# Kernel tuning notes

Hardware: AMD Instinct MI355X
Metric: run time of the kernel (lower is better)

## Reference

```python
import jax, jax.numpy as jnp
import numpy as np

DATA_DIM = 784
MANIFOLD_DIM = 16
HIDDEN = 256
BATCH = 131072


def setup_inputs() -> dict:
    key = jax.random.key(0)
    ks = jax.random.split(key, 10)
    s = lambda fan_in: 1.0 / np.sqrt(fan_in)
    return {
        "x_t": jax.random.normal(ks[0], (BATCH, DATA_DIM), dtype=jnp.float32),
        "t": jax.random.uniform(ks[1], (BATCH,), dtype=jnp.float32),
        # metric_net: Linear(784,256) -> ReLU -> Linear(256, 16*16)
        "W1": jax.random.uniform(ks[2], (DATA_DIM, HIDDEN), jnp.float32, -s(DATA_DIM), s(DATA_DIM)),
        "b1": jax.random.uniform(ks[3], (HIDDEN,), jnp.float32, -s(DATA_DIM), s(DATA_DIM)),
        "W2": jax.random.uniform(ks[4], (HIDDEN, MANIFOLD_DIM * MANIFOLD_DIM), jnp.float32, -s(HIDDEN), s(HIDDEN)),
        "b2": jax.random.uniform(ks[5], (MANIFOLD_DIM * MANIFOLD_DIM,), jnp.float32, -s(HIDDEN), s(HIDDEN)),
        # project_to_manifold: Linear(784, 16)
        "Wp": jax.random.uniform(ks[6], (DATA_DIM, MANIFOLD_DIM), jnp.float32, -s(DATA_DIM), s(DATA_DIM)),
        "bp": jax.random.uniform(ks[7], (MANIFOLD_DIM,), jnp.float32, -s(DATA_DIM), s(DATA_DIM)),
        # lift_from_manifold: Linear(16, 784)
        "Wl": jax.random.uniform(ks[8], (MANIFOLD_DIM, DATA_DIM), jnp.float32, -s(MANIFOLD_DIM), s(MANIFOLD_DIM)),
        "bl": jax.random.uniform(ks[9], (DATA_DIM,), jnp.float32, -s(MANIFOLD_DIM), s(MANIFOLD_DIM)),
    }


def reference(x_t, t, W1, b1, W2, b2, Wp, bp, Wl, bl):
    d = MANIFOLD_DIM
    # project_to_manifold
    xi = x_t @ Wp + bp  # [B, d]
    # metric_tensor: g = A A^T + 0.1 I, A = metric_net(x).reshape(B, d, d)
    h = jax.nn.relu(x_t @ W1 + b1)
    g_flat = h @ W2 + b2
    A = g_flat.reshape(-1, d, d)
    g = jnp.einsum('bik,bjk->bij', A, A) + 0.1 * jnp.eye(d, dtype=x_t.dtype)
    g_inv = jnp.linalg.inv(g)  # batched small 16x16 inverse
    # latent score: -xi / (t + eps)
    latent_score = -xi / (t[:, None] + 1e-6)
    riemannian_score = jnp.einsum('bij,bj->bi', g_inv, latent_score)
    score_data = riemannian_score @ Wl + bl  # [B, 784]
    return score_data
```

## Files before the change

### kernel.cpp

```cpp
#include <hip/hip_runtime.h>

typedef __attribute__((ext_vector_type(8))) short short8;
typedef __attribute__((ext_vector_type(4))) float f32x4;

#define NT   256
#define ROWS 32

#define W1T_PL  435200
#define W1T_COL 1600
#define W2T_OFF 870400
#define W2T_PL  131072
#define W2T_COL 512
#define WLT_OFF 1132544
#define WLT_PL  25088
#define WLT_COL 32

#define OFF_W0   0
#define OFF_W1   34816
#define OFF_H    34816
#define OFF_X0   69632
#define OFF_X1   73728
#define OFF_XIP  69632
#define OFF_YS   77824
#define LDS_SZ   79872

#define MFMA16(a,b,c) __builtin_amdgcn_mfma_f32_16x16x32_bf16(a,b,c,0,0,0)

__device__ __forceinline__ unsigned short bf16_rn(float x){
  unsigned u = __float_as_uint(x);
  return (unsigned short)((u + 0x7fffu + ((u >> 16) & 1u)) >> 16);
}
__device__ __forceinline__ float bf16f(unsigned short h){
  return __uint_as_float(((unsigned)h) << 16);
}

__device__ __forceinline__ void glds16(const void* g, void* s){
#if __has_builtin(__builtin_amdgcn_global_load_lds)
  __builtin_amdgcn_global_load_lds((const __attribute__((address_space(1))) void*)g,
                                   (__attribute__((address_space(3))) void*)s, 16, 0, 0);
#else
  const int lane = (int)(threadIdx.x & 63u);
  *(short8*)((char*)s + lane*16) = *(const short8*)((const char*)g);
#endif
}

__global__ __launch_bounds__(256)
void prep_w(const float* __restrict__ W1, const float* __restrict__ W2,
            const float* __restrict__ Wp, const float* __restrict__ Wl,
            unsigned short* __restrict__ ws)
{
  const int u = blockIdx.x * 256 + threadIdx.x;
  float v[8];
  int bh, blo;
  if (u < 27200) {
    int kg = u / 272, col = u - kg*272;
    #pragma unroll
    for (int j = 0; j < 8; ++j) {
      int k = kg*8 + j;
      v[j] = (k < 784) ? ((col < 256) ? W1[k*256 + col] : Wp[k*16 + (col-256)]) : 0.0f;
    }
    bh = col*800 + kg*8; blo = bh + 217600;
  } else if (u < 35392) {
    int q = u - 27200;
    int kg = q >> 8, col = q & 255;
    #pragma unroll
    for (int j = 0; j < 8; ++j) v[j] = W2[(kg*8+j)*256 + col];
    bh = 435200 + col*256 + kg*8; blo = bh + 65536;
  } else if (u < 36960) {
    int q = u - 35392;
    int kg = (q >= 784) ? 1 : 0; int col = q - kg*784;
    #pragma unroll
    for (int j = 0; j < 8; ++j) v[j] = Wl[(kg*8+j)*784 + col];
    bh = 566272 + col*16 + kg*8; blo = bh + 12544;
  } else return;
  short8 hv, lv;
  #pragma unroll
  for (int j = 0; j < 8; ++j) {
    unsigned short hh = bf16_rn(v[j]);
    hv[j] = (short)hh;
    lv[j] = (short)bf16_rn(v[j] - bf16f(hh));
  }
  *(short8*)&ws[bh]  = hv;
  *(short8*)&ws[blo] = lv;
}

__global__ __launch_bounds__(NT, 2)
void riemann_mfma(const float* __restrict__ x, const float* __restrict__ tvec,
                  const float* __restrict__ b1g, const float* __restrict__ b2g,
                  const float* __restrict__ bpg, const float* __restrict__ blg,
                  const char* __restrict__ wst, float* __restrict__ out)
{
  __shared__ __align__(16) char lds[LDS_SZ];
  const int tid = threadIdx.x;
  const int wv  = tid >> 6;
  const int l   = tid & 63;
  const int lr  = l & 15;
  const int lg  = l >> 4;
  const int row0 = (int)blockIdx.x * ROWS;

  const f32x4 Z4 = {0.f, 0.f, 0.f, 0.f};
  const short8 Z8 = {0,0,0,0,0,0,0,0};

  f32x4 acc[2][4];
  f32x4 xia[2];
  #pragma unroll
  for (int mt = 0; mt < 2; ++mt) {
    xia[mt] = Z4;
    #pragma unroll
    for (int nt = 0; nt < 4; ++nt) acc[mt][nt] = Z4;
  }

  const int xrow = tid >> 3;
  const int kq   = tid & 7;
  const int xwoff = xrow*64 + (((kq>>1) ^ ((xrow>>1)&3))<<4) + (kq&1)*8;

  auto loadX = [&](int ct)->f32x4 {
    f32x4 v = Z4;
    if (ct < 25) {
      int kb = ct*32 + kq*4;
      if (kb < 784) v = *(const f32x4*)(x + (long)(row0 + xrow)*784 + kb);
    }
    return v;
  };
  auto writeX = [&](const f32x4& xv, int slot){
    unsigned long long hq = 0, lq = 0;
    #pragma unroll
    for (int e = 0; e < 4; ++e) {
      unsigned short hh = bf16_rn(xv[e]);
      unsigned short ll = bf16_rn(xv[e] - bf16f(hh));
      hq |= ((unsigned long long)hh) << (16*e);
      lq |= ((unsigned long long)ll) << (16*e);
    }
    char* b = lds + (slot ? OFF_X1 : OFF_X0) + xwoff;
    *(unsigned long long*)b = hq;
    *(unsigned long long*)(b + 2048) = lq;
  };
  auto stageW1 = [&](int t, int slot){
    #pragma unroll
    for (int i2 = 0; i2 < 9; ++i2) {
      int i = wv + i2*4;
      if (i < 34) {
        int f = i*64 + l;
        int pl = (f >= 1088) ? 1 : 0;
        int r  = f - pl*1088;
        int col = r >> 2, kgp = r & 3;
        glds16(wst + pl*W1T_PL + col*W1T_COL + t*64 + ((kgp ^ ((col>>1)&3)) << 4),
               lds + (slot ? OFF_W1 : OFF_W0) + i*1024);
      }
    }
  };

  f32x4 xv0 = loadX(0);
  stageW1(0, 0);
  writeX(xv0, 0);
  f32x4 xv = loadX(1);
  __syncthreads();

  for (int t = 0; t < 25; ++t) {
    const int cur = t & 1, nxt = cur ^ 1;
    if (t < 24) {
      stageW1(t + 1, nxt);
      writeX(xv, nxt);
      xv = loadX(t + 2);
    }
    const char* Xb = lds + (cur ? OFF_X1 : OFF_X0);
    const char* Wb = lds + (cur ? OFF_W1 : OFF_W0);

    short8 af[2][2];
    #pragma unroll
    for (int mt = 0; mt < 2; ++mt) {
      int row = mt*16 + lr;
      int sl = lg ^ ((row>>1)&3);
      af[0][mt] = *(const short8*)(Xb +        row*64 + sl*16);
      af[1][mt] = *(const short8*)(Xb + 2048 + row*64 + sl*16);
    }
    short8 bfr[2][4];
    #pragma unroll
    for (int nt = 0; nt < 4; ++nt) {
      int col = wv*64 + nt*16 + lr;
      int sl = lg ^ ((col>>1)&3);
      bfr[0][nt] = *(const short8*)(Wb +         col*64 + sl*16);
      bfr[1][nt] = *(const short8*)(Wb + 17408 + col*64 + sl*16);
    }
    #pragma unroll
    for (int mt = 0; mt < 2; ++mt)
      #pragma unroll
      for (int nt = 0; nt < 4; ++nt) {
        acc[mt][nt] = MFMA16(af[0][mt], bfr[0][nt], acc[mt][nt]);
        acc[mt][nt] = MFMA16(af[0][mt], bfr[1][nt], acc[mt][nt]);
        acc[mt][nt] = MFMA16(af[1][mt], bfr[0][nt], acc[mt][nt]);
      }
    if ((t & 3) == wv) {
      int colx = 256 + lr;
      int slx = lg ^ ((colx>>1)&3);
      short8 bx0 = *(const short8*)(Wb +         colx*64 + slx*16);
      short8 bx1 = *(const short8*)(Wb + 17408 + colx*64 + slx*16);
      #pragma unroll
      for (int mt = 0; mt < 2; ++mt) {
        xia[mt] = MFMA16(af[0][mt], bx0, xia[mt]);
        xia[mt] = MFMA16(af[0][mt], bx1, xia[mt]);
        xia[mt] = MFMA16(af[1][mt], bx0, xia[mt]);
      }
    }
    __syncthreads();
  }

  {
    #pragma unroll
    for (int i2 = 0; i2 < 8; ++i2) {
      int i = wv + i2*4;
      int f = i*64 + l;
      int pl = f >> 10, r = f & 1023;
      int col = r >> 2, kgp = r & 3;
      glds16(wst + W2T_OFF + pl*W2T_PL + col*W2T_COL + 0*64 + ((kgp ^ ((col>>1)&3)) << 4),
             lds + OFF_W0 + i*1024);
    }
  }
  #pragma unroll
  for (int nt = 0; nt < 4; ++nt) {
    int col = wv*64 + nt*16 + lr;
    float b1v = b1g[col];
    #pragma unroll
    for (int mt = 0; mt < 2; ++mt)
      #pragma unroll
      for (int r = 0; r < 4; ++r) {
        int row = mt*16 + lg*4 + r;
        float v = acc[mt][nt][r] + b1v;
        v = v > 0.f ? v : 0.f;
        unsigned short hh = bf16_rn(v);
        unsigned short ll = bf16_rn(v - bf16f(hh));
        int bo = (row*512 + col*2) ^ ((row&7)<<4);
        *(unsigned short*)(lds + OFF_H +         bo) = hh;
        *(unsigned short*)(lds + OFF_H + 16384 + bo) = ll;
      }
  }
  #pragma unroll
  for (int mt = 0; mt < 2; ++mt)
    #pragma unroll
    for (int r = 0; r < 4; ++r) {
      int row = mt*16 + lg*4 + r;
      *(float*)(lds + OFF_XIP + wv*2048 + row*64 + lr*4) = xia[mt][r];
    }
  __syncthreads();

  f32x4 ac2[2][4];
  #pragma unroll
  for (int mt = 0; mt < 2; ++mt)
    #pragma unroll
    for (int nt = 0; nt < 4; ++nt) ac2[mt][nt] = Z4;

  for (int t = 0; t < 8; ++t) {
    short8 ah[2], alo[2];
    #pragma unroll
    for (int mt = 0; mt < 2; ++mt) {
      int row = mt*16 + lr;
      int bo = (row*512 + t*64 + lg*16) ^ ((row&7)<<4);
      ah[mt]  = *(const short8*)(lds + OFF_H +         bo);
      alo[mt] = *(const short8*)(lds + OFF_H + 16384 + bo);
    }
    short8 b2f[2][4];
    #pragma unroll
    for (int nt = 0; nt < 4; ++nt) {
      int col = wv*64 + nt*16 + lr;
      int sl = lg ^ ((col>>1)&3);
      b2f[0][nt] = *(const short8*)(lds + OFF_W0 +         col*64 + sl*16);
      b2f[1][nt] = *(const short8*)(lds + OFF_W0 + 16384 + col*64 + sl*16);
    }
    __syncthreads();
    if (t < 7) {
      #pragma unroll
      for (int i2 = 0; i2 < 8; ++i2) {
        int i = wv + i2*4;
        int f = i*64 + l;
        int pl = f >> 10, r = f & 1023;
        int col = r >> 2, kgp = r & 3;
        glds16(wst + W2T_OFF + pl*W2T_PL + col*W2T_COL + (t+1)*64 + ((kgp ^ ((col>>1)&3)) << 4),
               lds + OFF_W0 + i*1024);
      }
    }
    #pragma unroll
    for (int mt = 0; mt < 2; ++mt)
      #pragma unroll
      for (int nt = 0; nt < 4; ++nt) {
        ac2[mt][nt] = MFMA16(ah[mt],  b2f[0][nt], ac2[mt][nt]);
        ac2[mt][nt] = MFMA16(ah[mt],  b2f[1][nt], ac2[mt][nt]);
        ac2[mt][nt] = MFMA16(alo[mt], b2f[0][nt], ac2[mt][nt]);
      }
    __syncthreads();
  }
  #pragma unroll
  for (int nt = 0; nt < 4; ++nt) {
    int col = wv*64 + nt*16 + lr;
    float b2v = b2g[col];
    #pragma unroll
    for (int mt = 0; mt < 2; ++mt)
      #pragma unroll
      for (int r = 0; r < 4; ++r) {
        int row = mt*16 + lg*4 + r;
        *(float*)(lds + OFF_W0 + row*1024 + col*4) = ac2[mt][nt][r] + b2v;
      }
  }
  __syncthreads();

  const int grp = tid >> 4;
  const int j16 = tid & 15;
  float aA[16], aB[16];
  {
    const char* g0 = lds + OFF_W0 + grp*1024 + j16*64;
    const char* g1 = lds + OFF_W0 + (16+grp)*1024 + j16*64;
    *(f32x4*)&aA[0]  = *(const f32x4*)(g0);
    *(f32x4*)&aA[4]  = *(const f32x4*)(g0 + 16);
    *(f32x4*)&aA[8]  = *(const f32x4*)(g0 + 32);
    *(f32x4*)&aA[12] = *(const f32x4*)(g0 + 48);
    *(f32x4*)&aB[0]  = *(const f32x4*)(g1);
    *(f32x4*)&aB[4]  = *(const f32x4*)(g1 + 16);
    *(f32x4*)&aB[8]  = *(const f32x4*)(g1 + 32);
    *(f32x4*)&aB[12] = *(const f32x4*)(g1 + 48);
  }
  float bpv = bpg[j16];
  float xs0 = *(const float*)(lds + OFF_XIP +        grp*64 + j16*4)
            + *(const float*)(lds + OFF_XIP + 2048 + grp*64 + j16*4)
            + *(const float*)(lds + OFF_XIP + 4096 + grp*64 + j16*4)
            + *(const float*)(lds + OFF_XIP + 6144 + grp*64 + j16*4) + bpv;
  float xs1 = *(const float*)(lds + OFF_XIP +        (16+grp)*64 + j16*4)
            + *(const float*)(lds + OFF_XIP + 2048 + (16+grp)*64 + j16*4)
            + *(const float*)(lds + OFF_XIP + 4096 + (16+grp)*64 + j16*4)
            + *(const float*)(lds + OFF_XIP + 6144 + (16+grp)*64 + j16*4) + bpv;
  float rhs0 = -xs0 / (tvec[row0 + grp] + 1e-6f);
  float rhs1 = -xs1 / (tvec[row0 + 16 + grp] + 1e-6f);
  __syncthreads();

  {
    #pragma unroll
    for (int i2 = 0; i2 < 13; ++i2) {
      int i = wv + i2*4;
      if (i < 49) {
        int f = i*64 + l;
        int pl = (f >= 1568) ? 1 : 0;
        int r  = f - pl*1568;
        int col = r >> 1, kg = r & 1;
        glds16(wst + WLT_OFF + pl*WLT_PL + col*WLT_COL + kg*16,
               lds + OFF_W0 + i*1024);
      }
    }
  }
  {
    float rw[16];
    #pragma unroll
    for (int i = 0; i < 16; ++i) {
      float d = (i == j16) ? 0.1f : 0.0f;
      #pragma unroll
      for (int k = 0; k < 16; ++k) d += aA[k] * __shfl(aA[k], i, 16);
      rw[i] = d;
    }
    float rdv = 0.f;
    #pragma unroll
    for (int k = 0; k < 16; ++k) {
      float piv = __shfl(rw[k], k, 16);
      float rp = 1.0f / piv;
      float f = rw[k] * rp;
      f = (j16 == k) ? 0.0f : f;
      if (j16 == k) rdv = rp;
      #pragma unroll
      for (int q = k+1; q < 16; ++q)
        rw[q] -= f * __shfl(rw[q], k, 16);
      rhs0 -= f * __shfl(rhs0, k, 16);
    }
    float y = rhs0 * rdv;
    unsigned short yh = bf16_rn(y);
    unsigned short yl = bf16_rn(y - bf16f(yh));
    *(unsigned short*)(lds + OFF_YS +        grp*32 + j16*2) = yh;
    *(unsigned short*)(lds + OFF_YS + 1024 + grp*32 + j16*2) = yl;
  }
  {
    float rw[16];
    #pragma unroll
    for (int i = 0; i < 16; ++i) {
      float d = (i == j16) ? 0.1f : 0.0f;
      #pragma unroll
      for (int k = 0; k < 16; ++k) d += aB[k] * __shfl(aB[k], i, 16);
      rw[i] = d;
    }
    float rdv = 0.f;
    #pragma unroll
    for (int k = 0; k < 16; ++k) {
      float piv = __shfl(rw[k], k, 16);
      float rp = 1.0f / piv;
      float f = rw[k] * rp;
      f = (j16 == k) ? 0.0f : f;
      if (j16 == k) rdv = rp;
      #pragma unroll
      for (int q = k+1; q < 16; ++q)
        rw[q] -= f * __shfl(rw[q], k, 16);
      rhs1 -= f * __shfl(rhs1, k, 16);
    }
    float y = rhs1 * rdv;
    unsigned short yh = bf16_rn(y);
    unsigned short yl = bf16_rn(y - bf16f(yh));
    *(unsigned short*)(lds + OFF_YS +        (16+grp)*32 + j16*2) = yh;
    *(unsigned short*)(lds + OFF_YS + 1024 + (16+grp)*32 + j16*2) = yl;
  }
  __syncthreads();

  short8 ya[2][2];
  #pragma unroll
  for (int p = 0; p < 2; ++p)
    #pragma unroll
    for (int mt = 0; mt < 2; ++mt) {
      short8 v = Z8;
      if (lg < 2) v = *(const short8*)(lds + OFF_YS + p*1024 + (mt*16 + lr)*32 + lg*16);
      ya[p][mt] = v;
    }

  for (int nt = wv; nt < 49; nt += 4) {
    short8 w0 = Z8, w1v = Z8;
    if (lg < 2) {
      int col = nt*16 + lr;
      w0  = *(const short8*)(lds + OFF_W0 +         col*32 + lg*16);
      w1v = *(const short8*)(lds + OFF_W0 + 25088 + col*32 + lg*16);
    }
    float blv = blg[nt*16 + lr];
    #pragma unroll
    for (int mt = 0; mt < 2; ++mt) {
      f32x4 a5 = Z4;
      a5 = MFMA16(ya[0][mt], w0,  a5);
      a5 = MFMA16(ya[0][mt], w1v, a5);
      a5 = MFMA16(ya[1][mt], w0,  a5);
      #pragma unroll
      for (int r = 0; r < 4; ++r)
        out[(long)(row0 + mt*16 + lg*4 + r)*784 + nt*16 + lr] = a5[r] + blv;
    }
  }
}

extern "C" void kernel_launch(void* const* d_in, const int* in_sizes, int n_in,
                              void* d_out, int out_size, void* d_ws, size_t ws_size,
                              hipStream_t stream)
{
  (void)n_in; (void)out_size; (void)ws_size;
  const float* x  = (const float*)d_in[0];
  const float* t  = (const float*)d_in[1];
  const float* W1 = (const float*)d_in[2];
  const float* b1 = (const float*)d_in[3];
  const float* W2 = (const float*)d_in[4];
  const float* b2 = (const float*)d_in[5];
  const float* Wp = (const float*)d_in[6];
  const float* bp = (const float*)d_in[7];
  const float* Wl = (const float*)d_in[8];
  const float* bl = (const float*)d_in[9];
  float* out = (float*)d_out;
  const int B = in_sizes[1];

  hipLaunchKernelGGL(prep_w, dim3(145), dim3(256), 0, stream,
                     W1, W2, Wp, Wl, (unsigned short*)d_ws);
  hipLaunchKernelGGL(riemann_mfma, dim3(B / ROWS), dim3(NT), 0, stream,
                     x, t, b1, b2, bp, bl, (const char*)d_ws, out);
}
```

Before: 1.089 ms.

## Double block to 512 threads with explicit waitcnt/barrier pipelining and priority hints

Raises the workgroup to 8 waves, halving each wave's N-slice in both GEMM phases, splitting X loads into float2 per thread, and giving each thread one 16x16 solve instead of two. __syncthreads is replaced with manual vmcnt/lgkmcnt waits plus s_barrier so async global->LDS weight staging can stay in flight across iterations. MFMA sections are wrapped in s_setprio. The aim is more latency hiding and less per-thread serial solve work. The risks are wrong hand-counted vmcnt values and more barrier overhead.

```diff
diff --git a/kernel.cpp b/kernel.cpp
--- a/kernel.cpp
+++ b/kernel.cpp
@@ -2,8 +2,9 @@
 
 typedef __attribute__((ext_vector_type(8))) short short8;
 typedef __attribute__((ext_vector_type(4))) float f32x4;
-
-#define NT   256
+typedef __attribute__((ext_vector_type(2))) float f32x2;
+
+#define NT   512
 #define ROWS 32
 
 #define W1T_PL  435200
@@ -25,6 +26,9 @@
 #define LDS_SZ   79872
 
 #define MFMA16(a,b,c) __builtin_amdgcn_mfma_f32_16x16x32_bf16(a,b,c,0,0,0)
+#define WAITV(N) asm volatile("s_waitcnt vmcnt(" #N ")" ::: "memory")
+#define WAITL()  asm volatile("s_waitcnt lgkmcnt(0)" ::: "memory")
+#define SBAR()   __builtin_amdgcn_s_barrier()
 
 __device__ __forceinline__ unsigned short bf16_rn(float x){
   unsigned u = __float_as_uint(x);
@@ -84,7 +88,7 @@
   *(short8*)&ws[blo] = lv;
 }
 
-__global__ __launch_bounds__(NT, 2)
+__global__ __launch_bounds__(NT, 4)
 void riemann_mfma(const float* __restrict__ x, const float* __restrict__ tvec,
                   const float* __restrict__ b1g, const float* __restrict__ b2g,
                   const float* __restrict__ bpg, const float* __restrict__ blg,
@@ -101,44 +105,42 @@
   const f32x4 Z4 = {0.f, 0.f, 0.f, 0.f};
   const short8 Z8 = {0,0,0,0,0,0,0,0};
 
-  f32x4 acc[2][4];
+  f32x4 acc[2][2];
   f32x4 xia[2];
   #pragma unroll
   for (int mt = 0; mt < 2; ++mt) {
     xia[mt] = Z4;
     #pragma unroll
-    for (int nt = 0; nt < 4; ++nt) acc[mt][nt] = Z4;
-  }
-
-  const int xrow = tid >> 3;
-  const int kq   = tid & 7;
-  const int xwoff = xrow*64 + (((kq>>1) ^ ((xrow>>1)&3))<<4) + (kq&1)*8;
-
-  auto loadX = [&](int ct)->f32x4 {
-    f32x4 v = Z4;
+    for (int nt = 0; nt < 2; ++nt) acc[mt][nt] = Z4;
+  }
+
+  const int xrow = tid >> 4;
+  const int kq   = tid & 15;
+  const int xwoff = xrow*64 + ((((kq>>2) ^ ((xrow>>1)&3))) << 4) + (kq&3)*4;
+
+  auto loadX = [&](int ct)->f32x2 {
+    f32x2 v = {0.f, 0.f};
     if (ct < 25) {
-      int kb = ct*32 + kq*4;
-      if (kb < 784) v = *(const f32x4*)(x + (long)(row0 + xrow)*784 + kb);
+      int kb = ct*32 + kq*2;
+      int kbc = (kb < 784) ? kb : 782;
+      v = *(const f32x2*)(x + (long)(row0 + xrow)*784 + kbc);
+      if (kb >= 784) { v.x = 0.f; v.y = 0.f; }
     }
     return v;
   };
-  auto writeX = [&](const f32x4& xv, int slot){
-    unsigned long long hq = 0, lq = 0;
-    #pragma unroll
-    for (int e = 0; e < 4; ++e) {
-      unsigned short hh = bf16_rn(xv[e]);
-      unsigned short ll = bf16_rn(xv[e] - bf16f(hh));
-      hq |= ((unsigned long long)hh) << (16*e);
-      lq |= ((unsigned long long)ll) << (16*e);
-    }
+  auto writeX = [&](const f32x2& xv, int slot){
+    unsigned hw = (unsigned)bf16_rn(xv.x) | ((unsigned)bf16_rn(xv.y) << 16);
+    float rx = xv.x - bf16f(bf16_rn(xv.x));
+    float ry = xv.y - bf16f(bf16_rn(xv.y));
+    unsigned lw = (unsigned)bf16_rn(rx) | ((unsigned)bf16_rn(ry) << 16);
     char* b = lds + (slot ? OFF_X1 : OFF_X0) + xwoff;
-    *(unsigned long long*)b = hq;
-    *(unsigned long long*)(b + 2048) = lq;
+    *(unsigned*)b = hw;
+    *(unsigned*)(b + 2048) = lw;
   };
   auto stageW1 = [&](int t, int slot){
     #pragma unroll
-    for (int i2 = 0; i2 < 9; ++i2) {
-      int i = wv + i2*4;
+    for (int i2 = 0; i2 < 5; ++i2) {
+      int i = wv + i2*8;
       if (i < 34) {
         int f = i*64 + l;
         int pl = (f >= 1088) ? 1 : 0;
@@ -150,22 +152,29 @@
     }
   };
 
-  f32x4 xv0 = loadX(0);
   stageW1(0, 0);
+  __builtin_amdgcn_sched_barrier(0);
+  f32x2 xv0 = loadX(0);
   writeX(xv0, 0);
-  f32x4 xv = loadX(1);
+  f32x2 xv = loadX(1);
   __syncthreads();
 
   for (int t = 0; t < 25; ++t) {
     const int cur = t & 1, nxt = cur ^ 1;
     if (t < 24) {
       stageW1(t + 1, nxt);
+      __builtin_amdgcn_sched_barrier(0);
       writeX(xv, nxt);
       xv = loadX(t + 2);
     }
+    if (t < 23)       { if (wv < 2) { WAITV(6); } else { WAITV(5); } }
+    else if (t == 23) { if (wv < 2) { WAITV(5); } else { WAITV(4); } }
+    else              { WAITV(0); }
+    WAITL();
+    SBAR();
+
     const char* Xb = lds + (cur ? OFF_X1 : OFF_X0);
     const char* Wb = lds + (cur ? OFF_W1 : OFF_W0);
-
     short8 af[2][2];
     #pragma unroll
     for (int mt = 0; mt < 2; ++mt) {
@@ -174,18 +183,19 @@
       af[0][mt] = *(const short8*)(Xb +        row*64 + sl*16);
       af[1][mt] = *(const short8*)(Xb + 2048 + row*64 + sl*16);
     }
-    short8 bfr[2][4];
-    #pragma unroll
-    for (int nt = 0; nt < 4; ++nt) {
-      int col = wv*64 + nt*16 + lr;
+    short8 bfr[2][2];
+    #pragma unroll
+    for (int nt = 0; nt < 2; ++nt) {
+      int col = wv*32 + nt*16 + lr;
       int sl = lg ^ ((col>>1)&3);
       bfr[0][nt] = *(const short8*)(Wb +         col*64 + sl*16);
       bfr[1][nt] = *(const short8*)(Wb + 17408 + col*64 + sl*16);
     }
+    __builtin_amdgcn_s_setprio(1);
     #pragma unroll
     for (int mt = 0; mt < 2; ++mt)
       #pragma unroll
-      for (int nt = 0; nt < 4; ++nt) {
+      for (int nt = 0; nt < 2; ++nt) {
         acc[mt][nt] = MFMA16(af[0][mt], bfr[0][nt], acc[mt][nt]);
         acc[mt][nt] = MFMA16(af[0][mt], bfr[1][nt], acc[mt][nt]);
         acc[mt][nt] = MFMA16(af[1][mt], bfr[0][nt], acc[mt][nt]);
@@ -202,23 +212,28 @@
         xia[mt] = MFMA16(af[1][mt], bx0, xia[mt]);
       }
     }
-    __syncthreads();
-  }
-
-  {
-    #pragma unroll
-    for (int i2 = 0; i2 < 8; ++i2) {
-      int i = wv + i2*4;
+    __builtin_amdgcn_s_setprio(0);
+    WAITL();
+    SBAR();
+  }
+
+  auto stageW2 = [&](int t){
+    #pragma unroll
+    for (int i2 = 0; i2 < 4; ++i2) {
+      int i = wv + i2*8;
       int f = i*64 + l;
       int pl = f >> 10, r = f & 1023;
       int col = r >> 2, kgp = r & 3;
-      glds16(wst + W2T_OFF + pl*W2T_PL + col*W2T_COL + 0*64 + ((kgp ^ ((col>>1)&3)) << 4),
+      glds16(wst + W2T_OFF + pl*W2T_PL + col*W2T_COL + t*64 + ((kgp ^ ((col>>1)&3)) << 4),
              lds + OFF_W0 + i*1024);
     }
-  }
-  #pragma unroll
-  for (int nt = 0; nt < 4; ++nt) {
-    int col = wv*64 + nt*16 + lr;
+  };
+
+  stageW2(0);
+  __builtin_amdgcn_sched_barrier(0);
+  #pragma unroll
+  for (int nt = 0; nt < 2; ++nt) {
+    int col = wv*32 + nt*16 + lr;
     float b1v = b1g[col];
     #pragma unroll
     for (int mt = 0; mt < 2; ++mt)
@@ -234,20 +249,24 @@
         *(unsigned short*)(lds + OFF_H + 16384 + bo) = ll;
       }
   }
+  if (wv < 4) {
+    #pragma unroll
+    for (int mt = 0; mt < 2; ++mt)
+      #pragma unroll
+      for (int r = 0; r < 4; ++r) {
+        int row = mt*16 + lg*4 + r;
+        *(float*)(lds + OFF_XIP + wv*2048 + row*64 + lr*4) = xia[mt][r];
+      }
+  }
+  WAITV(0);
+  WAITL();
+  SBAR();
+
+  f32x4 ac2[2][2];
   #pragma unroll
   for (int mt = 0; mt < 2; ++mt)
     #pragma unroll
-    for (int r = 0; r < 4; ++r) {
-      int row = mt*16 + lg*4 + r;
-      *(float*)(lds + OFF_XIP + wv*2048 + row*64 + lr*4) = xia[mt][r];
-    }
-  __syncthreads();
-
-  f32x4 ac2[2][4];
-  #pragma unroll
-  for (int mt = 0; mt < 2; ++mt)
-    #pragma unroll
-    for (int nt = 0; nt < 4; ++nt) ac2[mt][nt] = Z4;
+    for (int nt = 0; nt < 2; ++nt) ac2[mt][nt] = Z4;
 
   for (int t = 0; t < 8; ++t) {
     short8 ah[2], alo[2];
@@ -258,39 +277,33 @@
       ah[mt]  = *(const short8*)(lds + OFF_H +         bo);
       alo[mt] = *(const short8*)(lds + OFF_H + 16384 + bo);
     }
-    short8 b2f[2][4];
-    #pragma unroll
-    for (int nt = 0; nt < 4; ++nt) {
-      int col = wv*64 + nt*16 + lr;
+    short8 b2f[2][2];
+    #pragma unroll
+    for (int nt = 0; nt < 2; ++nt) {
+      int col = wv*32 + nt*16 + lr;
       int sl = lg ^ ((col>>1)&3);
       b2f[0][nt] = *(const short8*)(lds + OFF_W0 +         col*64 + sl*16);
       b2f[1][nt] = *(const short8*)(lds + OFF_W0 + 16384 + col*64 + sl*16);
     }
-    __syncthreads();
-    if (t < 7) {
-      #pragma unroll
-      for (int i2 = 0; i2 < 8; ++i2) {
-        int i = wv + i2*4;
-        int f = i*64 + l;
-        int pl = f >> 10, r = f & 1023;
-        int col = r >> 2, kgp = r & 3;
-        glds16(wst + W2T_OFF + pl*W2T_PL + col*W2T_COL + (t+1)*64 + ((kgp ^ ((col>>1)&3)) << 4),
-               lds + OFF_W0 + i*1024);
-      }
-    }
+    WAITL();
+    SBAR();
+    if (t < 7) stageW2(t + 1);
+    __builtin_amdgcn_s_setprio(1);
     #pragma unroll
     for (int mt = 0; mt < 2; ++mt)
       #pragma unroll
-      for (int nt = 0; nt < 4; ++nt) {
+      for (int nt = 0; nt < 2; ++nt) {
         ac2[mt][nt] = MFMA16(ah[mt],  b2f[0][nt], ac2[mt][nt]);
         ac2[mt][nt] = MFMA16(ah[mt],  b2f[1][nt], ac2[mt][nt]);
         ac2[mt][nt] = MFMA16(alo[mt], b2f[0][nt], ac2[mt][nt]);
       }
-    __syncthreads();
-  }
-  #pragma unroll
-  for (int nt = 0; nt < 4; ++nt) {
-    int col = wv*64 + nt*16 + lr;
+    __builtin_amdgcn_s_setprio(0);
+    WAITV(0);
+    SBAR();
+  }
+  #pragma unroll
+  for (int nt = 0; nt < 2; ++nt) {
+    int col = wv*32 + nt*16 + lr;
     float b2v = b2g[col];
     #pragma unroll
     for (int mt = 0; mt < 2; ++mt)
@@ -300,40 +313,32 @@
         *(float*)(lds + OFF_W0 + row*1024 + col*4) = ac2[mt][nt][r] + b2v;
       }
   }
-  __syncthreads();
+  WAITL();
+  SBAR();
 
   const int grp = tid >> 4;
   const int j16 = tid & 15;
-  float aA[16], aB[16];
+  float a[16];
   {
-    const char* g0 = lds + OFF_W0 + grp*1024 + j16*64;
-    const char* g1 = lds + OFF_W0 + (16+grp)*1024 + j16*64;
-    *(f32x4*)&aA[0]  = *(const f32x4*)(g0);
-    *(f32x4*)&aA[4]  = *(const f32x4*)(g0 + 16);
-    *(f32x4*)&aA[8]  = *(const f32x4*)(g0 + 32);
-    *(f32x4*)&aA[12] = *(const f32x4*)(g0 + 48);
-    *(f32x4*)&aB[0]  = *(const f32x4*)(g1);
-    *(f32x4*)&aB[4]  = *(const f32x4*)(g1 + 16);
-    *(f32x4*)&aB[8]  = *(const f32x4*)(g1 + 32);
-    *(f32x4*)&aB[12] = *(const f32x4*)(g1 + 48);
-  }
-  float bpv = bpg[j16];
-  float xs0 = *(const float*)(lds + OFF_XIP +        grp*64 + j16*4)
-            + *(const float*)(lds + OFF_XIP + 2048 + grp*64 + j16*4)
-            + *(const float*)(lds + OFF_XIP + 4096 + grp*64 + j16*4)
-            + *(const float*)(lds + OFF_XIP + 6144 + grp*64 + j16*4) + bpv;
-  float xs1 = *(const float*)(lds + OFF_XIP +        (16+grp)*64 + j16*4)
-            + *(const float*)(lds + OFF_XIP + 2048 + (16+grp)*64 + j16*4)
-            + *(const float*)(lds + OFF_XIP + 4096 + (16+grp)*64 + j16*4)
-            + *(const float*)(lds + OFF_XIP + 6144 + (16+grp)*64 + j16*4) + bpv;
-  float rhs0 = -xs0 / (tvec[row0 + grp] + 1e-6f);
-  float rhs1 = -xs1 / (tvec[row0 + 16 + grp] + 1e-6f);
-  __syncthreads();
+    const char* gb = lds + OFF_W0 + grp*1024 + j16*64;
+    *(f32x4*)&a[0]  = *(const f32x4*)(gb);
+    *(f32x4*)&a[4]  = *(const f32x4*)(gb + 16);
+    *(f32x4*)&a[8]  = *(const f32x4*)(gb + 32);
+    *(f32x4*)&a[12] = *(const f32x4*)(gb + 48);
+  }
+  float xs = *(const float*)(lds + OFF_XIP +        grp*64 + j16*4)
+           + *(const float*)(lds + OFF_XIP + 2048 + grp*64 + j16*4)
+           + *(const float*)(lds + OFF_XIP + 4096 + grp*64 + j16*4)
+           + *(const float*)(lds + OFF_XIP + 6144 + grp*64 + j16*4)
+           + bpg[j16];
+  float rhs = -xs / (tvec[row0 + grp] + 1e-6f);
+  WAITL();
+  SBAR();
 
   {
     #pragma unroll
-    for (int i2 = 0; i2 < 13; ++i2) {
-      int i = wv + i2*4;
+    for (int i2 = 0; i2 < 7; ++i2) {
+      int i = wv + i2*8;
       if (i < 49) {
         int f = i*64 + l;
         int pl = (f >= 1568) ? 1 : 0;
@@ -344,13 +349,14 @@
       }
     }
   }
+  __builtin_amdgcn_sched_barrier(0);
   {
     float rw[16];
     #pragma unroll
     for (int i = 0; i < 16; ++i) {
       float d = (i == j16) ? 0.1f : 0.0f;
       #pragma unroll
-      for (int k = 0; k < 16; ++k) d += aA[k] * __shfl(aA[k], i, 16);
+      for (int k = 0; k < 16; ++k) d += a[k] * __shfl(a[k], i, 16);
       rw[i] = d;
     }
     float rdv = 0.f;
@@ -364,43 +370,17 @@
       #pragma unroll
       for (int q = k+1; q < 16; ++q)
         rw[q] -= f * __shfl(rw[q], k, 16);
-      rhs0 -= f * __shfl(rhs0, k, 16);
-    }
-    float y = rhs0 * rdv;
+      rhs -= f * __shfl(rhs, k, 16);
+    }
+    float y = rhs * rdv;
     unsigned short yh = bf16_rn(y);
     unsigned short yl = bf16_rn(y - bf16f(yh));
     *(unsigned short*)(lds + OFF_YS +        grp*32 + j16*2) = yh;
     *(unsigned short*)(lds + OFF_YS + 1024 + grp*32 + j16*2) = yl;
   }
-  {
-    float rw[16];
-    #pragma unroll
-    for (int i = 0; i < 16; ++i) {
-      float d = (i == j16) ? 0.1f : 0.0f;
-      #pragma unroll
-      for (int k = 0; k < 16; ++k) d += aB[k] * __shfl(aB[k], i, 16);
-      rw[i] = d;
-    }
-    float rdv = 0.f;
-    #pragma unroll
-    for (int k = 0; k < 16; ++k) {
-      float piv = __shfl(rw[k], k, 16);
-      float rp = 1.0f / piv;
-      float f = rw[k] * rp;
-      f = (j16 == k) ? 0.0f : f;
-      if (j16 == k) rdv = rp;
-      #pragma unroll
-      for (int q = k+1; q < 16; ++q)
-        rw[q] -= f * __shfl(rw[q], k, 16);
-      rhs1 -= f * __shfl(rhs1, k, 16);
-    }
-    float y = rhs1 * rdv;
-    unsigned short yh = bf16_rn(y);
-    unsigned short yl = bf16_rn(y - bf16f(yh));
-    *(unsigned short*)(lds + OFF_YS +        (16+grp)*32 + j16*2) = yh;
-    *(unsigned short*)(lds + OFF_YS + 1024 + (16+grp)*32 + j16*2) = yl;
-  }
-  __syncthreads();
+  WAITV(0);
+  WAITL();
+  SBAR();
 
   short8 ya[2][2];
   #pragma unroll
@@ -412,7 +392,7 @@
       ya[p][mt] = v;
     }
 
-  for (int nt = wv; nt < 49; nt += 4) {
+  for (int nt = wv; nt < 49; nt += 8) {
     short8 w0 = Z8, w1v = Z8;
     if (lg < 2) {
       int col = nt*16 + lr;
```

After: 1.107 ms. Within noise of the previous version (+1.7%).
